# Performance work log

Measured on AMD Instinct MI355X. Metric: run time of the kernel, lower is better.

The kernel has to match this reference:

```python
import jax, jax.numpy as jnp
import numpy as np

B = 32768   # batch
F = 32      # per-node feature dim
H = 256     # hidden width
M = 4       # modules per node
OUT = 8     # final output dim
INIT_W = 0.003
B_INIT = 0.1


def _lin(k, din, dout):
    # fanin_init-style uniform weights, bias filled with 0.1 (hidden layers)
    s = 1.0 / np.sqrt(din)
    W = jax.random.uniform(k, (M, din, dout), jnp.float32, -s, s)
    b = jnp.full((M, dout), B_INIT, jnp.float32)
    return W, b


def setup_inputs() -> dict:
    key = jax.random.key(0)
    ks = jax.random.split(key, 16)
    feats = jax.random.normal(ks[0], (B, 4 * F), jnp.float32)
    idx = jax.random.randint(ks[1], (B, 4), 0, M)
    onehots = jax.nn.one_hot(idx, M, dtype=jnp.float32).reshape(B, 4 * M)
    input_val = jnp.concatenate([feats, onehots], axis=1)  # [B,144]

    W00, b00 = _lin(ks[2], F, H)        # node0 post layer 0
    W01, b01 = _lin(ks[3], H, H)        # node0 post layer 1
    Wpre1, bpre1 = _lin(ks[4], F, H)    # node1 pre
    Wpost1, bpost1 = _lin(ks[5], 2 * H, H)  # node1 interface (prev 256 + own 256)
    Wpre2, bpre2 = _lin(ks[6], F, H)
    Wpost2, bpost2 = _lin(ks[7], 2 * H, H)
    Wpre3, bpre3 = _lin(ks[8], F, H)
    Wpost3, bpost3 = _lin(ks[9], 2 * H, H)
    # final output layer: uniform(-init_w, init_w) for W and b, identity act
    Wfin3 = jax.random.uniform(ks[10], (M, H, OUT), jnp.float32, -INIT_W, INIT_W)
    bfin3 = jax.random.uniform(ks[11], (M, OUT), jnp.float32, -INIT_W, INIT_W)
    return dict(input_val=input_val,
                W00=W00, b00=b00, W01=W01, b01=b01,
                Wpre1=Wpre1, bpre1=bpre1, Wpost1=Wpost1, bpost1=bpost1,
                Wpre2=Wpre2, bpre2=bpre2, Wpost2=Wpost2, bpost2=bpost2,
                Wpre3=Wpre3, bpre3=bpre3, Wpost3=Wpost3, bpost3=bpost3,
                Wfin3=Wfin3, bfin3=bfin3)


def _select(h, onehot):
    # per-row pick of the assigned module's output: [B,M,D],[B,M] -> [B,D]
    return jnp.einsum('bmo,bm->bo', h, onehot)


def reference(input_val, W00, b00, W01, b01,
              Wpre1, bpre1, Wpost1, bpost1,
              Wpre2, bpre2, Wpost2, bpost2,
              Wpre3, bpre3, Wpost3, bpost3,
              Wfin3, bfin3):
    feat = lambda j: input_val[:, j * F:(j + 1) * F]
    oh = lambda j: input_val[:, 4 * F + j * M: 4 * F + (j + 1) * M]

    # node 0: two hidden layers, module-dispatched (dense-all-modules + one-hot combine)
    h = jax.nn.relu(jnp.einsum('bi,mio->bmo', feat(0), W00) + b00)
    h = jax.nn.relu(jnp.einsum('bmi,mio->bmo', h, W01) + b01)
    x = _select(h, oh(0))  # [B,H]

    def node(x_prev, fj, ohj, Wpre, bpre, Wpost, bpost):
        hp = jax.nn.relu(jnp.einsum('bi,mio->bmo', fj, Wpre) + bpre)
        # interface layer consumes concat([x_prev, hp]); split the weight to
        # avoid materializing [B,M,2H]
        hq = jax.nn.relu(jnp.einsum('bi,mio->bmo', x_prev, Wpost[:, :H, :])
                         + jnp.einsum('bmi,mio->bmo', hp, Wpost[:, H:, :])
                         + bpost)
        return hq  # [B,M,H]

    x = _select(node(x, feat(1), oh(1), Wpre1, bpre1, Wpost1, bpost1), oh(1))
    x = _select(node(x, feat(2), oh(2), Wpre2, bpre2, Wpost2, bpost2), oh(2))

    h3 = node(x, feat(3), oh(3), Wpre3, bpre3, Wpost3, bpost3)  # [B,M,H]
    out = jnp.einsum('bmi,mio->bmo', h3, Wfin3) + bfin3          # final linear, identity act
    return _select(out, oh(3))  # [B,OUT]
```

## Files before the change

kernel.cpp:

```cpp
#include <hip/hip_runtime.h>

#define NB 32768
#define MAXTILE 768
#define XHS 536

typedef short s8v __attribute__((ext_vector_type(8)));
typedef short s4v __attribute__((ext_vector_type(4)));
typedef float f4v __attribute__((ext_vector_type(4)));
typedef unsigned short u16;
typedef unsigned short u16x4 __attribute__((ext_vector_type(4)));
typedef unsigned int u32;
typedef unsigned char u8;

__device__ __forceinline__ float bf2f(u16 u) { return __uint_as_float(((u32)u) << 16); }
__device__ __forceinline__ u16 f2bf(float f) {
    u32 x = __float_as_uint(f);
    x += 0x7FFFu + ((x >> 16) & 1u);
    return (u16)(x >> 16);
}
__device__ __forceinline__ s8v ld8(const u16* p) { return *reinterpret_cast<const s8v*>(p); }

#define MFMA16(a, b, c) __builtin_amdgcn_mfma_f32_16x16x32_bf16((a), (b), (c), 0, 0, 0)

__global__ __launch_bounds__(256) void probe_kernel(const void* __restrict__ input,
                                                    int* __restrict__ flagp,
                                                    int* __restrict__ counters)
{
    int tid = threadIdx.x;
    counters[tid] = 0;
    if (tid < 64) {
        u32 w = ((const u32*)input)[tid];
        u32 h0 = w & 0xFFFFu;
        u32 e0 = (h0 >> 7) & 0xFFu;
        bool plaus = (h0 == 0u) || (e0 >= 96u && e0 <= 143u);
        unsigned long long m = __ballot(plaus);
        if (tid == 0) *flagp = (__popcll(m) >= 48) ? 1 : 0;
    }
}

__global__ __launch_bounds__(256) void prepA_kernel(const void* __restrict__ inputv,
                                                    const int* __restrict__ flagp,
                                                    int* __restrict__ counters,
                                                    u8* __restrict__ keys)
{
    __shared__ int lcnt[256];
    int flag = *flagp;
    int tid = threadIdx.x;
    lcnt[tid] = 0;
    __syncthreads();
    int row = (blockIdx.x << 8) + tid;
    const u32* in32 = (const u32*)inputv;
    const u16* in16 = (const u16*)inputv;
    int key = 0;
#pragma unroll
    for (int j = 0; j < 4; j++) {
        int base = row * 144 + 128 + j * 4;
        u32 v1, v2, v3;
        if (flag) { v1 = in16[base + 1]; v2 = in16[base + 2]; v3 = in16[base + 3]; }
        else      { v1 = in32[base + 1]; v2 = in32[base + 2]; v3 = in32[base + 3]; }
        int m = v1 ? 1 : (v2 ? 2 : (v3 ? 3 : 0));
        key |= m << (j << 1);
    }
    keys[row] = (u8)key;
    atomicAdd(&lcnt[key], 1);
    __syncthreads();
    if (lcnt[tid]) atomicAdd(&counters[tid], lcnt[tid]);
}

__global__ __launch_bounds__(256) void scan_kernel(const int* __restrict__ counters,
                                                   int* __restrict__ cursors,
                                                   int4* __restrict__ tileInfo)
{
    __shared__ int sbuf[256];
    __shared__ int tot;
    int tid = threadIdx.x;
    int c = counters[tid];
    sbuf[tid] = c;
    __syncthreads();
    for (int off = 1; off < 256; off <<= 1) {
        int v = (tid >= off) ? sbuf[tid - off] : 0;
        __syncthreads();
        sbuf[tid] += v;
        __syncthreads();
    }
    int base = sbuf[tid] - c;
    cursors[tid] = base;
    int tiles = (c + 63) >> 6;
    __syncthreads();
    sbuf[tid] = tiles;
    __syncthreads();
    for (int off = 1; off < 256; off <<= 1) {
        int v = (tid >= off) ? sbuf[tid - off] : 0;
        __syncthreads();
        sbuf[tid] += v;
        __syncthreads();
    }
    int tbase = sbuf[tid] - tiles;
    if (tid == 255) tot = sbuf[255];
    __syncthreads();
    for (int t = 0; t < tiles; t++) {
        int rem = c - t * 64;
        tileInfo[tbase + t] = make_int4(tid, base + t * 64, rem > 64 ? 64 : rem, 0);
    }
    for (int i = tot + tid; i < MAXTILE; i += 256)
        tileInfo[i] = make_int4(0, 0, 0, 0);
}

__global__ __launch_bounds__(256) void prepB_kernel(const u8* __restrict__ keys,
                                                    int* __restrict__ cursors,
                                                    int* __restrict__ perm)
{
    __shared__ int lcnt[256];
    __shared__ int lbase[256];
    int tid = threadIdx.x;
    lcnt[tid] = 0;
    __syncthreads();
    int row = (blockIdx.x << 8) + tid;
    int key = keys[row];
    int loc = atomicAdd(&lcnt[key], 1);
    __syncthreads();
    if (lcnt[tid]) lbase[tid] = atomicAdd(&cursors[tid], lcnt[tid]);
    __syncthreads();
    perm[lbase[key] + loc] = row;
}

struct RepArgs {
    const void* W01; const void* Wp[3]; const void* pre[4]; const void* fin;
    const void* bias[9];
    u16 *rPre, *rW01, *rWp[3], *rFin, *cbias;
};

__global__ __launch_bounds__(256) void repack_kernel(const int* __restrict__ flagp, RepArgs R)
{
    __shared__ u16 T[8192];
    int flag = *flagp;
    int tid = threadIdx.x;
    int b = blockIdx.x;

    const void* src = nullptr; u16* dst = nullptr; int K = 0, k0 = 0, mrow = 0;
    if (b < 32) {
        int m = b >> 3, s = b & 7;
        src = R.W01; dst = R.rW01 + (m * 8 + s) * 8192; K = 256; k0 = s * 32; mrow = m;
    } else if (b < 224) {
        int idx = b - 32, mat = idx >> 6, r = idx & 63, m = r >> 4, s = r & 15;
        src = R.Wp[mat]; dst = R.rWp[mat] + (m * 16 + s) * 8192; K = 512; k0 = s * 32; mrow = m;
    } else if (b < 240) {
        int idx = b - 224, mat = idx >> 2, m = idx & 3;
        src = R.pre[mat]; dst = R.rPre + (mat * 4 + m) * 8192; K = 32; k0 = 0; mrow = m;
    } else if (b < 244) {
        int m = b - 240;
        const u16* s16 = (const u16*)R.fin;
        const float* s32 = (const float*)R.fin;
        for (int i = tid; i < 2048; i += 256) {
            int si = (m * 256 + (i >> 3)) * 8 + (i & 7);
            T[i] = flag ? s16[si] : f2bf(s32[si]);
        }
        __syncthreads();
        u16* d = R.rFin + m * 4096;
        for (int i = tid; i < 4096; i += 256) {
            int s = i >> 9, lane = (i >> 3) & 63, j = i & 7;
            int q = lane >> 4, l16 = lane & 15;
            int k = s * 32 + q * 8 + j;
            d[i] = (l16 < 8) ? T[k * 8 + l16] : (u16)0;
        }
        return;
    } else {
        const int sz[9] = {1024,1024,1024,1024,1024,1024,1024,1024,32};
        const int of[9] = {0,1024,2048,3072,4096,5120,6144,7168,8192};
        for (int i = tid; i < 8224; i += 256) {
            int t = i, e = 0;
            while (t >= sz[e]) { t -= sz[e]; e++; }
            R.cbias[of[e] + t] = flag ? ((const u16*)R.bias[e])[t]
                                      : f2bf(((const float*)R.bias[e])[t]);
        }
        return;
    }

    const u16* s16 = (const u16*)src;
    const float* s32 = (const float*)src;
    for (int i = tid; i < 8192; i += 256) {
        int k = i >> 8, n = i & 255;
        int srcIdx = (mrow * K + k0 + k) * 256 + n;
        T[i] = flag ? s16[srcIdx] : f2bf(s32[srcIdx]);
    }
    __syncthreads();
    for (int i = tid; i < 8192; i += 256) {
        int mt = i >> 9, lane = (i >> 3) & 63, j = i & 7;
        int k = ((lane >> 4) << 3) + j, n = (mt << 4) + (lane & 15);
        dst[i] = T[(k << 8) + n];
    }
}

struct MainP { const u16 *rPre, *rW01, *rWp1, *rWp2, *rWp3, *rFin, *cbias; };

__global__ __launch_bounds__(512, 4) void main_kernel(
    const void* __restrict__ inRaw, const int* __restrict__ flagp,
    const int* __restrict__ perm, const int4* __restrict__ tileInfo,
    MainP P, void* __restrict__ outp)
{
    __shared__ __align__(16) u16 xh[64 * XHS];
    __shared__ int rowids[64];

    int tid = threadIdx.x;
    int lane = tid & 63, w = tid >> 6, quad = lane >> 4, l16 = lane & 15;

    int4 ti = tileInfo[blockIdx.x];
    int key = ti.x, ppos = ti.y, cntIn = ti.z;
    if (cntIn <= 0) return;
    int flag = *flagp;

    if (tid < 64) {
        int g = tid < cntIn ? tid : cntIn - 1;
        rowids[tid] = perm[ppos + g];
    }
    __syncthreads();
    int rows[4];
#pragma unroll
    for (int nt = 0; nt < 4; nt++) rows[nt] = rowids[nt * 16 + l16];

    const u16* mainW[4] = {P.rW01, P.rWp1, P.rWp2, P.rWp3};
    const u16* in16 = (const u16*)inRaw;
    const float* in32 = (const float*)inRaw;

    for (int node = 0; node < 4; node++) {
        int m = (key >> (node << 1)) & 3;

        s8v fb[4];
#pragma unroll
        for (int nt = 0; nt < 4; nt++) {
            int off = rows[nt] * 144 + (node << 5) + (quad << 3);
            if (flag) fb[nt] = ld8(in16 + off);
            else {
                f4v f0 = *(const f4v*)(in32 + off);
                f4v f1 = *(const f4v*)(in32 + off + 4);
                s8v r;
#pragma unroll
                for (int j = 0; j < 4; j++) { r[j] = (short)f2bf(f0[j]); r[4 + j] = (short)f2bf(f1[j]); }
                fb[nt] = r;
            }
        }

        const u16* preB = P.rPre + ((node << 2) + m) * 8192;
#pragma unroll
        for (int ci = 0; ci < 2; ci++) {
            int mt = (w << 1) + ci;
            s8v a = ld8(preB + mt * 512 + lane * 8);
            u16x4 bv = *(const u16x4*)(P.cbias + node * 2048 + m * 256 + mt * 16 + quad * 4);
            f4v bias;
#pragma unroll
            for (int r = 0; r < 4; r++) bias[r] = bf2f(bv[r]);
#pragma unroll
            for (int nt = 0; nt < 4; nt++) {
                f4v c = MFMA16(a, fb[nt], bias);
                s4v p;
#pragma unroll
                for (int r = 0; r < 4; r++) { float v = c[r] > 0.f ? c[r] : 0.f; p[r] = (short)f2bf(v); }
                *(s4v*)&xh[(nt * 16 + l16) * XHS + 256 + mt * 16 + quad * 4] = p;
            }
        }
        __syncthreads();

        int s0 = node ? 0 : 8;
        const u16* WB = mainW[node] + m * (node ? 16 : 8) * 8192;
        f4v acc[2][4];
        {
            u16x4 b0 = *(const u16x4*)(P.cbias + node * 2048 + 1024 + m * 256 + ((w << 1) + 0) * 16 + quad * 4);
            u16x4 b1 = *(const u16x4*)(P.cbias + node * 2048 + 1024 + m * 256 + ((w << 1) + 1) * 16 + quad * 4);
            f4v f0, f1;
#pragma unroll
            for (int r = 0; r < 4; r++) { f0[r] = bf2f(b0[r]); f1[r] = bf2f(b1[r]); }
#pragma unroll
            for (int nt = 0; nt < 4; nt++) { acc[0][nt] = f0; acc[1][nt] = f1; }
        }
        {
            s8v A0 = ld8(WB + (w << 1) * 512 + lane * 8);
            s8v A1 = ld8(WB + ((w << 1) + 1) * 512 + lane * 8);
#pragma unroll
            for (int s = s0; s < 16; s++) {
                s8v nA0 = A0, nA1 = A1;
                if (s + 1 < 16) {
                    const u16* nb = WB + (s + 1 - s0) * 8192;
                    nA0 = ld8(nb + (w << 1) * 512 + lane * 8);
                    nA1 = ld8(nb + ((w << 1) + 1) * 512 + lane * 8);
                }
#pragma unroll
                for (int nt = 0; nt < 4; nt++) {
                    s8v B = ld8(&xh[(nt * 16 + l16) * XHS + s * 32 + quad * 8]);
                    acc[0][nt] = MFMA16(A0, B, acc[0][nt]);
                    acc[1][nt] = MFMA16(A1, B, acc[1][nt]);
                }
                A0 = nA0;
                A1 = nA1;
            }
        }
        __syncthreads();

#pragma unroll
        for (int ci = 0; ci < 2; ci++) {
            int mt = (w << 1) + ci;
#pragma unroll
            for (int nt = 0; nt < 4; nt++) {
                s4v p;
#pragma unroll
                for (int r = 0; r < 4; r++) {
                    float v = acc[ci][nt][r]; v = v > 0.f ? v : 0.f;
                    p[r] = (short)f2bf(v);
                }
                *(s4v*)&xh[(nt * 16 + l16) * XHS + mt * 16 + quad * 4] = p;
            }
        }
    }
    __syncthreads();

    if (w < 4) {
        int m3 = (key >> 6) & 3;
        f4v c;
#pragma unroll
        for (int r = 0; r < 4; r++)
            c[r] = (quad < 2) ? bf2f(P.cbias[8192 + m3 * 8 + quad * 4 + r]) : 0.f;
#pragma unroll
        for (int s = 0; s < 8; s++) {
            s8v A = ld8(P.rFin + m3 * 4096 + s * 512 + lane * 8);
            s8v B = ld8(&xh[(w * 16 + l16) * XHS + s * 32 + quad * 8]);
            c = MFMA16(A, B, c);
        }
        int bidx = w * 16 + l16;
        if (quad < 2 && bidx < cntIn) {
            int row = rowids[bidx];
            if (flag) {
                s4v p;
#pragma unroll
                for (int r = 0; r < 4; r++) p[r] = (short)f2bf(c[r]);
                *(s4v*)((u16*)outp + row * 8 + quad * 4) = p;
            } else {
                *(f4v*)((float*)outp + row * 8 + quad * 4) = c;
            }
        }
    }
}

extern "C" void kernel_launch(void* const* d_in, const int* in_sizes, int n_in,
                              void* d_out, int out_size, void* d_ws, size_t ws_size,
                              hipStream_t stream)
{
    (void)in_sizes; (void)n_in; (void)out_size;
    const void* input  = d_in[0];
    const void* W00    = d_in[1];
    const void* b00    = d_in[2];
    const void* W01    = d_in[3];
    const void* b01    = d_in[4];
    const void* Wpre1  = d_in[5];
    const void* bpre1  = d_in[6];
    const void* Wpost1 = d_in[7];
    const void* bpost1 = d_in[8];
    const void* Wpre2  = d_in[9];
    const void* bpre2  = d_in[10];
    const void* Wpost2 = d_in[11];
    const void* bpost2 = d_in[12];
    const void* Wpre3  = d_in[13];
    const void* bpre3  = d_in[14];
    const void* Wpost3 = d_in[15];
    const void* bpost3 = d_in[16];
    const void* Wfin   = d_in[17];
    const void* bfin   = d_in[18];

    char* base = (char*)d_ws;
    size_t off = 0;
    auto alloc = [&](size_t bytes) -> char* {
        char* p = base + off;
        off += (bytes + 255) & ~(size_t)255;
        return p;
    };
    int*  flagp    = (int*)alloc(4);
    int*  counters = (int*)alloc(256 * 4);
    int*  cursors  = (int*)alloc(256 * 4);
    u8*   keys     = (u8*)alloc(NB);
    int4* tileInfo = (int4*)alloc(MAXTILE * 16);
    int*  perm     = (int*)alloc((size_t)NB * 4);
    u16*  cbias    = (u16*)alloc(8224 * 2);
    u16*  rPre     = (u16*)alloc(131072 * 2);
    u16*  rW01     = (u16*)alloc(262144 * 2);
    u16*  rWp1     = (u16*)alloc(524288 * 2);
    u16*  rWp2     = (u16*)alloc(524288 * 2);
    u16*  rWp3     = (u16*)alloc(524288 * 2);
    u16*  rFin     = (u16*)alloc(16384 * 2);
    if (off > ws_size) return;

    probe_kernel<<<1, 256, 0, stream>>>(input, flagp, counters);
    prepA_kernel<<<128, 256, 0, stream>>>(input, flagp, counters, keys);
    scan_kernel<<<1, 256, 0, stream>>>(counters, cursors, tileInfo);
    prepB_kernel<<<128, 256, 0, stream>>>(keys, cursors, perm);

    RepArgs R;
    R.W01 = W01; R.Wp[0] = Wpost1; R.Wp[1] = Wpost2; R.Wp[2] = Wpost3;
    R.pre[0] = W00; R.pre[1] = Wpre1; R.pre[2] = Wpre2; R.pre[3] = Wpre3;
    R.fin = Wfin;
    R.bias[0] = b00;   R.bias[1] = b01;
    R.bias[2] = bpre1; R.bias[3] = bpost1;
    R.bias[4] = bpre2; R.bias[5] = bpost2;
    R.bias[6] = bpre3; R.bias[7] = bpost3;
    R.bias[8] = bfin;
    R.rPre = rPre; R.rW01 = rW01;
    R.rWp[0] = rWp1; R.rWp[1] = rWp2; R.rWp[2] = rWp3;
    R.rFin = rFin; R.cbias = cbias;
    repack_kernel<<<245, 256, 0, stream>>>(flagp, R);

    MainP P;
    P.rPre = rPre; P.rW01 = rW01; P.rWp1 = rWp1; P.rWp2 = rWp2; P.rWp3 = rWp3;
    P.rFin = rFin; P.cbias = cbias;
    main_kernel<<<MAXTILE, 512, 0, stream>>>(input, flagp, perm, tileInfo, P, d_out);
}
```

Before: 200.3 us.

## Fuse prep kernels, shrink row tiles to 48, deepen weight prefetch

Merges the probe, key-count, scan and weight-repack kernels into one prep kernel that uses a last-block-done counter to run the scan, cutting several launches. The main kernel now processes 48-row tiles (3 MFMA column tiles) instead of 64 and raises the launch-bounds occupancy hint from 4 to 6. Weight A-fragments are prefetched three k-steps ahead. The first half of the interface GEMM runs before the barrier that publishes the pre-layer output, so it can overlap with the other waves. Smaller tiles mean more blocks and more total weight reads. The extra occupancy may also force register spills.

```diff
diff --git a/kernel.cpp b/kernel.cpp
--- a/kernel.cpp
+++ b/kernel.cpp
@@ -1,7 +1,9 @@
 #include <hip/hip_runtime.h>
 
 #define NB 32768
-#define MAXTILE 768
+#define MAXTILE 1024
+#define ROWS 48
+#define NT 3
 #define XHS 536
 
 typedef short s8v __attribute__((ext_vector_type(8)));
@@ -22,106 +24,16 @@
 
 #define MFMA16(a, b, c) __builtin_amdgcn_mfma_f32_16x16x32_bf16((a), (b), (c), 0, 0, 0)
 
-__global__ __launch_bounds__(256) void probe_kernel(const void* __restrict__ input,
-                                                    int* __restrict__ flagp,
-                                                    int* __restrict__ counters)
+__device__ __forceinline__ void detect_flag(const void* input, int tid, int* shflag)
 {
-    int tid = threadIdx.x;
-    counters[tid] = 0;
     if (tid < 64) {
         u32 w = ((const u32*)input)[tid];
         u32 h0 = w & 0xFFFFu;
         u32 e0 = (h0 >> 7) & 0xFFu;
         bool plaus = (h0 == 0u) || (e0 >= 96u && e0 <= 143u);
         unsigned long long m = __ballot(plaus);
-        if (tid == 0) *flagp = (__popcll(m) >= 48) ? 1 : 0;
-    }
-}
-
-__global__ __launch_bounds__(256) void prepA_kernel(const void* __restrict__ inputv,
-                                                    const int* __restrict__ flagp,
-                                                    int* __restrict__ counters,
-                                                    u8* __restrict__ keys)
-{
-    __shared__ int lcnt[256];
-    int flag = *flagp;
-    int tid = threadIdx.x;
-    lcnt[tid] = 0;
-    __syncthreads();
-    int row = (blockIdx.x << 8) + tid;
-    const u32* in32 = (const u32*)inputv;
-    const u16* in16 = (const u16*)inputv;
-    int key = 0;
-#pragma unroll
-    for (int j = 0; j < 4; j++) {
-        int base = row * 144 + 128 + j * 4;
-        u32 v1, v2, v3;
-        if (flag) { v1 = in16[base + 1]; v2 = in16[base + 2]; v3 = in16[base + 3]; }
-        else      { v1 = in32[base + 1]; v2 = in32[base + 2]; v3 = in32[base + 3]; }
-        int m = v1 ? 1 : (v2 ? 2 : (v3 ? 3 : 0));
-        key |= m << (j << 1);
-    }
-    keys[row] = (u8)key;
-    atomicAdd(&lcnt[key], 1);
-    __syncthreads();
-    if (lcnt[tid]) atomicAdd(&counters[tid], lcnt[tid]);
-}
-
-__global__ __launch_bounds__(256) void scan_kernel(const int* __restrict__ counters,
-                                                   int* __restrict__ cursors,
-                                                   int4* __restrict__ tileInfo)
-{
-    __shared__ int sbuf[256];
-    __shared__ int tot;
-    int tid = threadIdx.x;
-    int c = counters[tid];
-    sbuf[tid] = c;
-    __syncthreads();
-    for (int off = 1; off < 256; off <<= 1) {
-        int v = (tid >= off) ? sbuf[tid - off] : 0;
-        __syncthreads();
-        sbuf[tid] += v;
-        __syncthreads();
-    }
-    int base = sbuf[tid] - c;
-    cursors[tid] = base;
-    int tiles = (c + 63) >> 6;
-    __syncthreads();
-    sbuf[tid] = tiles;
-    __syncthreads();
-    for (int off = 1; off < 256; off <<= 1) {
-        int v = (tid >= off) ? sbuf[tid - off] : 0;
-        __syncthreads();
-        sbuf[tid] += v;
-        __syncthreads();
-    }
-    int tbase = sbuf[tid] - tiles;
-    if (tid == 255) tot = sbuf[255];
-    __syncthreads();
-    for (int t = 0; t < tiles; t++) {
-        int rem = c - t * 64;
-        tileInfo[tbase + t] = make_int4(tid, base + t * 64, rem > 64 ? 64 : rem, 0);
-    }
-    for (int i = tot + tid; i < MAXTILE; i += 256)
-        tileInfo[i] = make_int4(0, 0, 0, 0);
-}
-
-__global__ __launch_bounds__(256) void prepB_kernel(const u8* __restrict__ keys,
-                                                    int* __restrict__ cursors,
-                                                    int* __restrict__ perm)
-{
-    __shared__ int lcnt[256];
-    __shared__ int lbase[256];
-    int tid = threadIdx.x;
-    lcnt[tid] = 0;
-    __syncthreads();
-    int row = (blockIdx.x << 8) + tid;
-    int key = keys[row];
-    int loc = atomicAdd(&lcnt[key], 1);
-    __syncthreads();
-    if (lcnt[tid]) lbase[tid] = atomicAdd(&cursors[tid], lcnt[tid]);
-    __syncthreads();
-    perm[lbase[key] + loc] = row;
+        if (tid == 0) *shflag = (__popcll(m) >= 48) ? 1 : 0;
+    }
 }
 
 struct RepArgs {
@@ -130,25 +42,93 @@
     u16 *rPre, *rW01, *rWp[3], *rFin, *cbias;
 };
 
-__global__ __launch_bounds__(256) void repack_kernel(const int* __restrict__ flagp, RepArgs R)
+__global__ __launch_bounds__(256) void prep_kernel(const void* __restrict__ inputv,
+                                                   int* __restrict__ counters,
+                                                   u8* __restrict__ keys,
+                                                   int* __restrict__ cursors,
+                                                   int4* __restrict__ tileInfo,
+                                                   RepArgs R)
 {
+    __shared__ int lcnt[256];
     __shared__ u16 T[8192];
-    int flag = *flagp;
+    __shared__ int shmisc;
     int tid = threadIdx.x;
     int b = blockIdx.x;
-
+    detect_flag(inputv, tid, &shmisc);
+    __syncthreads();
+    int flag = shmisc;
+
+    if (b < 128) {
+        lcnt[tid] = 0;
+        __syncthreads();
+        int row = (b << 8) + tid;
+        const u32* in32 = (const u32*)inputv;
+        const u16* in16 = (const u16*)inputv;
+        int key = 0;
+#pragma unroll
+        for (int j = 0; j < 4; j++) {
+            int base = row * 144 + 128 + j * 4;
+            u32 v1, v2, v3;
+            if (flag) { v1 = in16[base + 1]; v2 = in16[base + 2]; v3 = in16[base + 3]; }
+            else      { v1 = in32[base + 1]; v2 = in32[base + 2]; v3 = in32[base + 3]; }
+            int m = v1 ? 1 : (v2 ? 2 : (v3 ? 3 : 0));
+            key |= m << (j << 1);
+        }
+        keys[row] = (u8)key;
+        atomicAdd(&lcnt[key], 1);
+        __syncthreads();
+        if (lcnt[tid]) atomicAdd(&counters[tid], lcnt[tid]);
+        __threadfence();
+        __syncthreads();
+        if (tid == 0) shmisc = atomicAdd(&counters[256], 1);
+        __syncthreads();
+        if (shmisc == 127) {
+            int c = __hip_atomic_load(&counters[tid], __ATOMIC_RELAXED, __HIP_MEMORY_SCOPE_AGENT);
+            lcnt[tid] = c;
+            __syncthreads();
+            for (int off = 1; off < 256; off <<= 1) {
+                int v = (tid >= off) ? lcnt[tid - off] : 0;
+                __syncthreads();
+                lcnt[tid] += v;
+                __syncthreads();
+            }
+            int base = lcnt[tid] - c;
+            cursors[tid] = base;
+            int tiles = (c + ROWS - 1) / ROWS;
+            __syncthreads();
+            lcnt[tid] = tiles;
+            __syncthreads();
+            for (int off = 1; off < 256; off <<= 1) {
+                int v = (tid >= off) ? lcnt[tid - off] : 0;
+                __syncthreads();
+                lcnt[tid] += v;
+                __syncthreads();
+            }
+            int tbase = lcnt[tid] - tiles;
+            int tot = lcnt[255];
+            for (int t = 0; t < tiles; t++) {
+                int rem = c - t * ROWS;
+                tileInfo[tbase + t] = make_int4(tid, base + t * ROWS, rem > ROWS ? ROWS : rem, 0);
+            }
+            for (int i = tot + tid; i < MAXTILE; i += 256)
+                tileInfo[i] = make_int4(0, 0, 0, 0);
+        }
+        return;
+    }
+
+    int rb = b - 128;
     const void* src = nullptr; u16* dst = nullptr; int K = 0, k0 = 0, mrow = 0;
-    if (b < 32) {
-        int m = b >> 3, s = b & 7;
+    if (rb < 32) {
+        int m = rb >> 3, s = rb & 7;
         src = R.W01; dst = R.rW01 + (m * 8 + s) * 8192; K = 256; k0 = s * 32; mrow = m;
-    } else if (b < 224) {
-        int idx = b - 32, mat = idx >> 6, r = idx & 63, m = r >> 4, s = r & 15;
+    } else if (rb < 224) {
+        int idx = rb - 32, mat = idx >> 6, r = idx & 63, m = r >> 4, s = r & 15;
         src = R.Wp[mat]; dst = R.rWp[mat] + (m * 16 + s) * 8192; K = 512; k0 = s * 32; mrow = m;
-    } else if (b < 240) {
-        int idx = b - 224, mat = idx >> 2, m = idx & 3;
+    } else if (rb < 240) {
+        int idx = rb - 224, mat = idx >> 2, m = idx & 3;
         src = R.pre[mat]; dst = R.rPre + (mat * 4 + m) * 8192; K = 32; k0 = 0; mrow = m;
-    } else if (b < 244) {
-        int m = b - 240;
+    } else if (rb < 244) {
+        int m = rb - 240;
         const u16* s16 = (const u16*)R.fin;
         const float* s32 = (const float*)R.fin;
         for (int i = tid; i < 2048; i += 256) {
@@ -175,7 +155,6 @@
         }
         return;
     }
-
     const u16* s16 = (const u16*)src;
     const float* s32 = (const float*)src;
     for (int i = tid; i < 8192; i += 256) {
@@ -191,15 +170,34 @@
     }
 }
 
+__global__ __launch_bounds__(256) void prepB_kernel(const u8* __restrict__ keys,
+                                                    int* __restrict__ cursors,
+                                                    int* __restrict__ perm)
+{
+    __shared__ int lcnt[256];
+    __shared__ int lbase[256];
+    int tid = threadIdx.x;
+    lcnt[tid] = 0;
+    __syncthreads();
+    int row = (blockIdx.x << 8) + tid;
+    int key = keys[row];
+    int loc = atomicAdd(&lcnt[key], 1);
+    __syncthreads();
+    if (lcnt[tid]) lbase[tid] = atomicAdd(&cursors[tid], lcnt[tid]);
+    __syncthreads();
+    perm[lbase[key] + loc] = row;
+}
+
 struct MainP { const u16 *rPre, *rW01, *rWp1, *rWp2, *rWp3, *rFin, *cbias; };
 
-__global__ __launch_bounds__(512, 4) void main_kernel(
-    const void* __restrict__ inRaw, const int* __restrict__ flagp,
+__global__ __launch_bounds__(512, 6) void main_kernel(
+    const void* __restrict__ inRaw,
     const int* __restrict__ perm, const int4* __restrict__ tileInfo,
     MainP P, void* __restrict__ outp)
 {
-    __shared__ __align__(16) u16 xh[64 * XHS];
-    __shared__ int rowids[64];
+    __shared__ __align__(16) u16 xh[ROWS * XHS];
+    __shared__ int rowids[ROWS];
+    __shared__ int shflag;
 
     int tid = threadIdx.x;
     int lane = tid & 63, w = tid >> 6, quad = lane >> 4, l16 = lane & 15;
@@ -207,27 +205,54 @@
     int4 ti = tileInfo[blockIdx.x];
     int key = ti.x, ppos = ti.y, cntIn = ti.z;
     if (cntIn <= 0) return;
-    int flag = *flagp;
-
-    if (tid < 64) {
+
+    detect_flag(inRaw, tid, &shflag);
+    if (tid < ROWS) {
         int g = tid < cntIn ? tid : cntIn - 1;
         rowids[tid] = perm[ppos + g];
     }
     __syncthreads();
-    int rows[4];
-#pragma unroll
-    for (int nt = 0; nt < 4; nt++) rows[nt] = rowids[nt * 16 + l16];
-
-    const u16* mainW[4] = {P.rW01, P.rWp1, P.rWp2, P.rWp3};
+    int flag = shflag;
+    int rows[NT];
+#pragma unroll
+    for (int nt = 0; nt < NT; nt++) rows[nt] = rowids[nt * 16 + l16];
+
     const u16* in16 = (const u16*)inRaw;
     const float* in32 = (const float*)inRaw;
+    int mt0 = w << 1, mt1 = mt0 + 1;
+
+    f4v acc0[NT], acc1[NT];
+
+    auto gemm8 = [&](const u16* Abase, int ks0) {
+        s8v A0a = ld8(Abase + (0 * 16 + mt0) * 512 + lane * 8);
+        s8v A1a = ld8(Abase + (0 * 16 + mt1) * 512 + lane * 8);
+        s8v A0b = ld8(Abase + (1 * 16 + mt0) * 512 + lane * 8);
+        s8v A1b = ld8(Abase + (1 * 16 + mt1) * 512 + lane * 8);
+        s8v A0c = ld8(Abase + (2 * 16 + mt0) * 512 + lane * 8);
+        s8v A1c = ld8(Abase + (2 * 16 + mt1) * 512 + lane * 8);
+#pragma unroll
+        for (int s = 0; s < 8; s++) {
+            s8v c0 = A0a, c1 = A1a;
+            A0a = A0b; A1a = A1b; A0b = A0c; A1b = A1c;
+            if (s < 5) {
+                A0c = ld8(Abase + ((s + 3) * 16 + mt0) * 512 + lane * 8);
+                A1c = ld8(Abase + ((s + 3) * 16 + mt1) * 512 + lane * 8);
+            }
+#pragma unroll
+            for (int nt = 0; nt < NT; nt++) {
+                s8v B = ld8(&xh[(nt * 16 + l16) * XHS + (ks0 + s) * 32 + quad * 8]);
+                acc0[nt] = MFMA16(c0, B, acc0[nt]);
+                acc1[nt] = MFMA16(c1, B, acc1[nt]);
+            }
+        }
+    };
 
     for (int node = 0; node < 4; node++) {
         int m = (key >> (node << 1)) & 3;
 
-        s8v fb[4];
-#pragma unroll
-        for (int nt = 0; nt < 4; nt++) {
+        s8v fb[NT];
+#pragma unroll
+        for (int nt = 0; nt < NT; nt++) {
             int off = rows[nt] * 144 + (node << 5) + (quad << 3);
             if (flag) fb[nt] = ld8(in16 + off);
             else {
@@ -243,14 +268,14 @@
         const u16* preB = P.rPre + ((node << 2) + m) * 8192;
 #pragma unroll
         for (int ci = 0; ci < 2; ci++) {
-            int mt = (w << 1) + ci;
+            int mt = mt0 + ci;
             s8v a = ld8(preB + mt * 512 + lane * 8);
             u16x4 bv = *(const u16x4*)(P.cbias + node * 2048 + m * 256 + mt * 16 + quad * 4);
             f4v bias;
 #pragma unroll
             for (int r = 0; r < 4; r++) bias[r] = bf2f(bv[r]);
 #pragma unroll
-            for (int nt = 0; nt < 4; nt++) {
+            for (int nt = 0; nt < NT; nt++) {
                 f4v c = MFMA16(a, fb[nt], bias);
                 s4v p;
 #pragma unroll
@@ -258,61 +283,40 @@
                 *(s4v*)&xh[(nt * 16 + l16) * XHS + 256 + mt * 16 + quad * 4] = p;
             }
         }
-        __syncthreads();
-
-        int s0 = node ? 0 : 8;
-        const u16* WB = mainW[node] + m * (node ? 16 : 8) * 8192;
-        f4v acc[2][4];
+
         {
-            u16x4 b0 = *(const u16x4*)(P.cbias + node * 2048 + 1024 + m * 256 + ((w << 1) + 0) * 16 + quad * 4);
-            u16x4 b1 = *(const u16x4*)(P.cbias + node * 2048 + 1024 + m * 256 + ((w << 1) + 1) * 16 + quad * 4);
+            u16x4 b0 = *(const u16x4*)(P.cbias + node * 2048 + 1024 + m * 256 + mt0 * 16 + quad * 4);
+            u16x4 b1 = *(const u16x4*)(P.cbias + node * 2048 + 1024 + m * 256 + mt1 * 16 + quad * 4);
             f4v f0, f1;
 #pragma unroll
             for (int r = 0; r < 4; r++) { f0[r] = bf2f(b0[r]); f1[r] = bf2f(b1[r]); }
 #pragma unroll
-            for (int nt = 0; nt < 4; nt++) { acc[0][nt] = f0; acc[1][nt] = f1; }
-        }
-        {
-            s8v A0 = ld8(WB + (w << 1) * 512 + lane * 8);
-            s8v A1 = ld8(WB + ((w << 1) + 1) * 512 + lane * 8);
-#pragma unroll
-            for (int s = s0; s < 16; s++) {
-                s8v nA0 = A0, nA1 = A1;
-                if (s + 1 < 16) {
-                    const u16* nb = WB + (s + 1 - s0) * 8192;
-                    nA0 = ld8(nb + (w << 1) * 512 + lane * 8);
-                    nA1 = ld8(nb + ((w << 1) + 1) * 512 + lane * 8);
-                }
-#pragma unroll
-                for (int nt = 0; nt < 4; nt++) {
-                    s8v B = ld8(&xh[(nt * 16 + l16) * XHS + s * 32 + quad * 8]);
-                    acc[0][nt] = MFMA16(A0, B, acc[0][nt]);
-                    acc[1][nt] = MFMA16(A1, B, acc[1][nt]);
-                }
-                A0 = nA0;
-                A1 = nA1;
-            }
-        }
-        __syncthreads();
+            for (int nt = 0; nt < NT; nt++) { acc0[nt] = f0; acc1[nt] = f1; }
+        }
+
+        const u16* WB = node ? ((node == 1 ? P.rWp1 : (node == 2 ? P.rWp2 : P.rWp3)) + m * 16 * 8192)
+                             : (P.rW01 + m * 8 * 8192);
+
+        if (node) gemm8(WB, 0);
+        __syncthreads();
+        gemm8(node ? (WB + 8 * 8192) : WB, 8);
 
 #pragma unroll
         for (int ci = 0; ci < 2; ci++) {
-            int mt = (w << 1) + ci;
-#pragma unroll
-            for (int nt = 0; nt < 4; nt++) {
+            int mt = mt0 + ci;
+#pragma unroll
+            for (int nt = 0; nt < NT; nt++) {
+                f4v a = ci ? acc1[nt] : acc0[nt];
                 s4v p;
 #pragma unroll
-                for (int r = 0; r < 4; r++) {
-                    float v = acc[ci][nt][r]; v = v > 0.f ? v : 0.f;
-                    p[r] = (short)f2bf(v);
-                }
+                for (int r = 0; r < 4; r++) { float v = a[r] > 0.f ? a[r] : 0.f; p[r] = (short)f2bf(v); }
                 *(s4v*)&xh[(nt * 16 + l16) * XHS + mt * 16 + quad * 4] = p;
             }
         }
-    }
-    __syncthreads();
-
-    if (w < 4) {
+        __syncthreads();
+    }
+
+    if (w < NT) {
         int m3 = (key >> 6) & 3;
         f4v c;
 #pragma unroll
@@ -371,8 +375,7 @@
         off += (bytes + 255) & ~(size_t)255;
         return p;
     };
-    int*  flagp    = (int*)alloc(4);
-    int*  counters = (int*)alloc(256 * 4);
+    int*  counters = (int*)alloc(257 * 4);
     int*  cursors  = (int*)alloc(256 * 4);
     u8*   keys     = (u8*)alloc(NB);
     int4* tileInfo = (int4*)alloc(MAXTILE * 16);
@@ -386,10 +389,7 @@
     u16*  rFin     = (u16*)alloc(16384 * 2);
     if (off > ws_size) return;
 
-    probe_kernel<<<1, 256, 0, stream>>>(input, flagp, counters);
-    prepA_kernel<<<128, 256, 0, stream>>>(input, flagp, counters, keys);
-    scan_kernel<<<1, 256, 0, stream>>>(counters, cursors, tileInfo);
-    prepB_kernel<<<128, 256, 0, stream>>>(keys, cursors, perm);
+    hipMemsetAsync(counters, 0, 257 * 4, stream);
 
     RepArgs R;
     R.W01 = W01; R.Wp[0] = Wpost1; R.Wp[1] = Wpost2; R.Wp[2] = Wpost3;
@@ -403,10 +403,12 @@
     R.rPre = rPre; R.rW01 = rW01;
     R.rWp[0] = rWp1; R.rWp[1] = rWp2; R.rWp[2] = rWp3;
     R.rFin = rFin; R.cbias = cbias;
-    repack_kernel<<<245, 256, 0, stream>>>(flagp, R);
+
+    prep_kernel<<<373, 256, 0, stream>>>(input, counters, keys, cursors, tileInfo, R);
+    prepB_kernel<<<128, 256, 0, stream>>>(keys, cursors, perm);
 
     MainP P;
     P.rPre = rPre; P.rW01 = rW01; P.rWp1 = rWp1; P.rWp2 = rWp2; P.rWp3 = rWp3;
     P.rFin = rFin; P.cbias = cbias;
-    main_kernel<<<MAXTILE, 512, 0, stream>>>(input, flagp, perm, tileInfo, P, d_out);
-}
+    main_kernel<<<MAXTILE, 512, 0, stream>>>(input, perm, tileInfo, P, d_out);
+}
```

Measured after the change: 209.5 us. 1.05x slower.
